# Performance work log

Measured on AMD Instinct MI355X. Metric: run time of the kernel, lower is better.

Reference implementation:

```python
import jax, jax.numpy as jnp
import numpy as np

FEAT = 1152
HID = [768, 512, 256]
WS = 32
LN_EPS = 1e-5


def _ln(x, g, b):
    mu = jnp.mean(x, axis=-1, keepdims=True)
    var = jnp.mean(jnp.square(x - mu), axis=-1, keepdims=True)
    return (x - mu) * jax.lax.rsqrt(var + LN_EPS) * g + b


def setup_inputs() -> dict:
    key = jax.random.key(0)
    ks = jax.random.split(key, 16)
    B, N, C = 8, 9216, FEAT

    def lin(k, din, dout):
        s = 1.0 / np.sqrt(din)
        k1, k2 = jax.random.split(k)
        return (jax.random.uniform(k1, (din, dout), jnp.float32, -s, s),
                jax.random.uniform(k2, (dout,), jnp.float32, -s, s))

    x = jax.random.normal(ks[0], (B, N, C), jnp.float32)
    W1, b1 = lin(ks[1], C, HID[0])
    W2, b2 = lin(ks[2], HID[0], HID[1])
    W3, b3 = lin(ks[3], HID[1], HID[2])
    Wo, bo = lin(ks[4], HID[2], C)
    red = C // 8
    ca_w1, ca_b1 = lin(ks[5], C, red)
    ca_w2, ca_b2 = lin(ks[6], red, C)
    return {
        "x": x,
        "W1": W1, "b1": b1, "g1": jnp.ones((HID[0],)), "be1": jnp.zeros((HID[0],)),
        "W2": W2, "b2": b2, "g2": jnp.ones((HID[1],)), "be2": jnp.zeros((HID[1],)),
        "W3": W3, "b3": b3, "g3": jnp.ones((HID[2],)), "be3": jnp.zeros((HID[2],)),
        "Wo": Wo, "bo": bo,
        "ca_w1": ca_w1, "ca_b1": ca_b1, "ca_w2": ca_w2, "ca_b2": ca_b2,
    }


def reference(x, W1, b1, g1, be1, W2, b2, g2, be2, W3, b3, g3, be3,
              Wo, bo, ca_w1, ca_b1, ca_w2, ca_b2):
    B, N, C = x.shape
    # projection + hidden blocks: Linear -> GELU(exact) -> LayerNorm
    h = _ln(jax.nn.gelu(x @ W1 + b1, approximate=False), g1, be1)
    h = _ln(jax.nn.gelu(h @ W2 + b2, approximate=False), g2, be2)
    h = _ln(jax.nn.gelu(h @ W3 + b3, approximate=False), g3, be3)
    y = h @ Wo + bo  # (B, N, C)
    # SE channel attention: global avg-pool over seq, 1x1 convs (=linear)
    pooled = jnp.mean(y, axis=1)                                  # (B, C)
    s = jax.nn.relu(pooled @ ca_w1 + ca_b1)                       # (B, C/8)
    s = jax.nn.sigmoid(s @ ca_w2 + ca_b2)                         # (B, C)
    y = y * s[:, None, :]
    # block-diagonal local self-attention, window = WS, scale 1/sqrt(C)
    nw = N // WS
    yw = y.reshape(B, nw, WS, C)
    scores = jnp.einsum('bwqc,bwkc->bwqk', yw, yw) / jnp.sqrt(jnp.asarray(C, y.dtype))
    attn = jax.nn.softmax(scores, axis=-1)
    out = jnp.einsum('bwqk,bwkc->bwqc', attn, yw)
    return out.reshape(B, N, C)
```

## Files before the change

### kernel.cpp

```cpp
#include <hip/hip_runtime.h>
#include <cstdint>
#include <cstddef>

typedef __bf16 bf16;
typedef __bf16 bf16x8 __attribute__((ext_vector_type(8)));
typedef float f32x4 __attribute__((ext_vector_type(4)));

__device__ __forceinline__ void gload_lds16(const bf16* g, bf16* l) {
    __builtin_amdgcn_global_load_lds((const __attribute__((address_space(1))) void*)g,
                                     (__attribute__((address_space(3))) void*)l, 16, 0, 0);
}

__global__ void cvt_f32_bf16_kernel(const float* __restrict__ in, bf16* __restrict__ outp, size_t n) {
    const size_t i = ((size_t)blockIdx.x * 256 + threadIdx.x) * 8;
    if (i >= n) return;
    const float4 a = *(const float4*)(in + i);
    const float4 b = *(const float4*)(in + i + 4);
    bf16x8 o;
    o[0] = (bf16)a.x; o[1] = (bf16)a.y; o[2] = (bf16)a.z; o[3] = (bf16)a.w;
    o[4] = (bf16)b.x; o[5] = (bf16)b.y; o[6] = (bf16)b.z; o[7] = (bf16)b.w;
    *(bf16x8*)(outp + i) = o;
}

__global__ void wtrans_all_kernel(const float* __restrict__ W1, bf16* __restrict__ T1,
                                  const float* __restrict__ W2, bf16* __restrict__ T2,
                                  const float* __restrict__ W3, bf16* __restrict__ T3,
                                  const float* __restrict__ Wo, bf16* __restrict__ To)
{
    __shared__ bf16 tile[64][65];
    const int id = blockIdx.x;
    const int t = threadIdx.x;
    const float* W; bf16* T; int K, N, kb, nb;
    if (id < 216)      { W = W1; T = T1; K = 1152; N = 768;  const int r = id;       kb = r % 18; nb = r / 18; }
    else if (id < 312) { W = W2; T = T2; K = 768;  N = 512;  const int r = id - 216; kb = r % 12; nb = r / 12; }
    else if (id < 344) { W = W3; T = T3; K = 512;  N = 256;  const int r = id - 312; kb = r % 8;  nb = r / 8;  }
    else               { W = Wo; T = To; K = 256;  N = 1152; const int r = id - 344; kb = r % 4;  nb = r / 4;  }
    const int k0 = kb << 6;
    const int n0 = nb << 6;
#pragma unroll
    for (int i = 0; i < 16; ++i) {
        const int flat = i * 256 + t;
        const int r = flat >> 6;
        const int c = flat & 63;
        tile[c][r] = (bf16)W[(size_t)(k0 + r) * N + n0 + c];
    }
    __syncthreads();
#pragma unroll
    for (int i = 0; i < 16; ++i) {
        const int flat = i * 256 + t;
        const int r = flat >> 6;
        const int c = flat & 63;
        T[(size_t)(n0 + r) * K + k0 + c] = tile[r][c];
    }
}

__device__ __forceinline__ int xcd_swz(int bid, int nwg) {
    return (bid & 7) * (nwg >> 3) + (bid >> 3);
}

__global__ void gemm_bf16_kernel(const bf16* __restrict__ A, const bf16* __restrict__ Bt,
                                 const float* __restrict__ bias, bf16* __restrict__ C,
                                 int K, int N, int nx, int do_gelu)
{
    __shared__ bf16 Alds[128 * 64];
    __shared__ bf16 Blds[128 * 64];
    const int t = threadIdx.x;
    const int w = t >> 6;
    const int l = t & 63;
    const int l15 = l & 15, l4 = l >> 4;
    const int wgid = xcd_swz(blockIdx.x, gridDim.x);
    const int mblk = wgid / nx;
    const int nblk = wgid - mblk * nx;
    const int m0 = mblk << 7;
    const int n0 = nblk << 7;
    const int wm = (w >> 1) << 6;
    const int wn = (w & 1) << 6;

    f32x4 acc[4][4] = {};

    int sr[4], sg[4];
#pragma unroll
    for (int i = 0; i < 4; ++i) {
        const int flat = i * 256 + t;
        sr[i] = flat >> 3;
        sg[i] = ((flat & 7) ^ (sr[i] & 7)) << 3;
    }

    for (int k0 = 0; k0 < K; k0 += 64) {
#pragma unroll
        for (int i = 0; i < 4; ++i) {
            gload_lds16(A + (size_t)(m0 + sr[i]) * K + (k0 + sg[i]),
                        &Alds[(size_t)(i * 256 + (w << 6)) << 3]);
            gload_lds16(Bt + (size_t)(n0 + sr[i]) * K + (k0 + sg[i]),
                        &Blds[(size_t)(i * 256 + (w << 6)) << 3]);
        }
        __syncthreads();
#pragma unroll
        for (int kk = 0; kk < 2; ++kk) {
            bf16x8 af[4], bfv[4];
#pragma unroll
            for (int i = 0; i < 4; ++i) {
                const int r = wm + (i << 4) + l15;
                const int g = (kk << 2) + l4;
                af[i] = *(const bf16x8*)&Alds[(r << 6) + ((g ^ (r & 7)) << 3)];
                const int rn = wn + (i << 4) + l15;
                bfv[i] = *(const bf16x8*)&Blds[(rn << 6) + ((g ^ (rn & 7)) << 3)];
            }
#pragma unroll
            for (int i = 0; i < 4; ++i)
#pragma unroll
                for (int j = 0; j < 4; ++j)
                    acc[i][j] = __builtin_amdgcn_mfma_f32_16x16x32_bf16(af[i], bfv[j], acc[i][j], 0, 0, 0);
        }
        __syncthreads();
    }

#pragma unroll
    for (int i = 0; i < 4; ++i) {
        const int mb = m0 + wm + (i << 4) + (l4 << 2);
#pragma unroll
        for (int j = 0; j < 4; ++j) {
            const int col = n0 + wn + (j << 4) + l15;
            const float bv = bias[col];
#pragma unroll
            for (int r = 0; r < 4; ++r) {
                float v = acc[i][j][r] + bv;
                if (do_gelu) v = 0.5f * v * (1.0f + erff(v * 0.70710678118654752f));
                C[(size_t)(mb + r) * N + col] = (bf16)v;
            }
        }
    }
}

__global__ void ln768_kernel(bf16* __restrict__ H, const float* __restrict__ g,
                             const float* __restrict__ be)
{
    const int t = threadIdx.x;
    const int rloc = t >> 7;
    const int u = t & 127;
    bf16* hp = H + ((size_t)blockIdx.x * 2 + rloc) * 768;
    float v[8];
    float s1 = 0.f, s2 = 0.f;
    if (u < 96) {
        const bf16x8 hv = *(const bf16x8*)(hp + u * 8);
#pragma unroll
        for (int e = 0; e < 8; ++e) { v[e] = (float)hv[e]; s1 += v[e]; s2 += v[e] * v[e]; }
    }
#pragma unroll
    for (int m = 1; m < 64; m <<= 1) { s1 += __shfl_xor(s1, m, 64); s2 += __shfl_xor(s2, m, 64); }
    __shared__ float red[8];
    const int w = t >> 6;
    if ((t & 63) == 0) { red[w] = s1; red[w + 4] = s2; }
    __syncthreads();
    const int wb = rloc << 1;
    s1 = red[wb] + red[wb + 1];
    s2 = red[wb + 4] + red[wb + 5];
    const float mu = s1 * (1.0f / 768.0f);
    const float rstd = rsqrtf(s2 * (1.0f / 768.0f) - mu * mu + 1e-5f);
    if (u < 96) {
        const float4 g0 = *(const float4*)(g + u * 8);
        const float4 g1 = *(const float4*)(g + u * 8 + 4);
        const float4 b0 = *(const float4*)(be + u * 8);
        const float4 b1 = *(const float4*)(be + u * 8 + 4);
        bf16x8 o;
        o[0] = (bf16)((v[0] - mu) * rstd * g0.x + b0.x);
        o[1] = (bf16)((v[1] - mu) * rstd * g0.y + b0.y);
        o[2] = (bf16)((v[2] - mu) * rstd * g0.z + b0.z);
        o[3] = (bf16)((v[3] - mu) * rstd * g0.w + b0.w);
        o[4] = (bf16)((v[4] - mu) * rstd * g1.x + b1.x);
        o[5] = (bf16)((v[5] - mu) * rstd * g1.y + b1.y);
        o[6] = (bf16)((v[6] - mu) * rstd * g1.z + b1.z);
        o[7] = (bf16)((v[7] - mu) * rstd * g1.w + b1.w);
        *(bf16x8*)(hp + u * 8) = o;
    }
}

__global__ void ln512_kernel(bf16* __restrict__ H, const float* __restrict__ g,
                             const float* __restrict__ be)
{
    const int t = threadIdx.x;
    const int w = t >> 6, l = t & 63;
    bf16* hp = H + ((size_t)blockIdx.x * 4 + w) * 512;
    const bf16x8 hv = *(const bf16x8*)(hp + l * 8);
    float v[8];
    float s1 = 0.f, s2 = 0.f;
#pragma unroll
    for (int e = 0; e < 8; ++e) { v[e] = (float)hv[e]; s1 += v[e]; s2 += v[e] * v[e]; }
#pragma unroll
    for (int m = 1; m < 64; m <<= 1) { s1 += __shfl_xor(s1, m, 64); s2 += __shfl_xor(s2, m, 64); }
    const float mu = s1 * (1.0f / 512.0f);
    const float rstd = rsqrtf(s2 * (1.0f / 512.0f) - mu * mu + 1e-5f);
    const float4 g0 = *(const float4*)(g + l * 8);
    const float4 g1 = *(const float4*)(g + l * 8 + 4);
    const float4 b0 = *(const float4*)(be + l * 8);
    const float4 b1 = *(const float4*)(be + l * 8 + 4);
    bf16x8 o;
    o[0] = (bf16)((v[0] - mu) * rstd * g0.x + b0.x);
    o[1] = (bf16)((v[1] - mu) * rstd * g0.y + b0.y);
    o[2] = (bf16)((v[2] - mu) * rstd * g0.z + b0.z);
    o[3] = (bf16)((v[3] - mu) * rstd * g0.w + b0.w);
    o[4] = (bf16)((v[4] - mu) * rstd * g1.x + b1.x);
    o[5] = (bf16)((v[5] - mu) * rstd * g1.y + b1.y);
    o[6] = (bf16)((v[6] - mu) * rstd * g1.z + b1.z);
    o[7] = (bf16)((v[7] - mu) * rstd * g1.w + b1.w);
    *(bf16x8*)(hp + l * 8) = o;
}

__global__ void ln256_kernel(bf16* __restrict__ H, const float* __restrict__ g,
                             const float* __restrict__ be)
{
    const int t = threadIdx.x;
    const int rloc = t >> 5, l = t & 31;
    bf16* hp = H + ((size_t)blockIdx.x * 8 + rloc) * 256;
    const bf16x8 hv = *(const bf16x8*)(hp + l * 8);
    float v[8];
    float s1 = 0.f, s2 = 0.f;
#pragma unroll
    for (int e = 0; e < 8; ++e) { v[e] = (float)hv[e]; s1 += v[e]; s2 += v[e] * v[e]; }
#pragma unroll
    for (int m = 1; m < 32; m <<= 1) { s1 += __shfl_xor(s1, m, 64); s2 += __shfl_xor(s2, m, 64); }
    const float mu = s1 * (1.0f / 256.0f);
    const float rstd = rsqrtf(s2 * (1.0f / 256.0f) - mu * mu + 1e-5f);
    const float4 g0 = *(const float4*)(g + l * 8);
    const float4 g1 = *(const float4*)(g + l * 8 + 4);
    const float4 b0 = *(const float4*)(be + l * 8);
    const float4 b1 = *(const float4*)(be + l * 8 + 4);
    bf16x8 o;
    o[0] = (bf16)((v[0] - mu) * rstd * g0.x + b0.x);
    o[1] = (bf16)((v[1] - mu) * rstd * g0.y + b0.y);
    o[2] = (bf16)((v[2] - mu) * rstd * g0.z + b0.z);
    o[3] = (bf16)((v[3] - mu) * rstd * g0.w + b0.w);
    o[4] = (bf16)((v[4] - mu) * rstd * g1.x + b1.x);
    o[5] = (bf16)((v[5] - mu) * rstd * g1.y + b1.y);
    o[6] = (bf16)((v[6] - mu) * rstd * g1.z + b1.z);
    o[7] = (bf16)((v[7] - mu) * rstd * g1.w + b1.w);
    *(bf16x8*)(hp + l * 8) = o;
}

__global__ void pool1_kernel(const bf16* __restrict__ Y, float* __restrict__ ppart) {
    const int c = blockIdx.x * 128 + threadIdx.x;
    const int nc = blockIdx.y;
    const int b = blockIdx.z;
    const bf16* yp = Y + ((size_t)b * 9216 + (size_t)nc * 256) * 1152 + c;
    float s = 0.f;
#pragma unroll 4
    for (int i = 0; i < 256; ++i) s += (float)yp[(size_t)i * 1152];
    ppart[((size_t)b * 36 + nc) * 1152 + c] = s;
}

__global__ void se_kernel(const float* __restrict__ ppart,
                          const float* __restrict__ w1, const float* __restrict__ b1,
                          const float* __restrict__ w2, const float* __restrict__ b2,
                          float* __restrict__ sbuf)
{
    const int b = blockIdx.x, t = threadIdx.x;
    __shared__ float p[1152];
    __shared__ float t1[144];
    for (int c = t; c < 1152; c += 256) {
        float s = 0.f;
#pragma unroll
        for (int j = 0; j < 36; ++j) s += ppart[((size_t)b * 36 + j) * 1152 + c];
        p[c] = s * (1.0f / 9216.0f);
    }
    __syncthreads();
    if (t < 144) {
        float a = b1[t];
        for (int k = 0; k < 1152; ++k) a += p[k] * w1[k * 144 + t];
        t1[t] = a > 0.f ? a : 0.f;
    }
    __syncthreads();
    for (int c = t; c < 1152; c += 256) {
        float a = b2[c];
#pragma unroll 8
        for (int k = 0; k < 144; ++k) a += t1[k] * w2[k * 1152 + c];
        sbuf[b * 1152 + c] = 1.0f / (1.0f + expf(-a));
    }
}

__device__ __forceinline__ int fswz(int r) { return (r & 7) ^ ((r >> 3) & 3); }

#define OSTG_STRIDE 388

__global__ void attn_kernel(const bf16* __restrict__ Y, const float* __restrict__ sbuf,
                            float* __restrict__ out)
{
    __shared__ __align__(16) char smem[24576 + 49664 + 2048];
    bf16*  yw   = (bf16*)smem;
    float* SpF  = (float*)(smem + 24576);
    float* ostg = (float*)(smem + 24576);
    bf16*  P    = (bf16*)(smem + 24576 + 49664);

    const int t = threadIdx.x;
    const int w = t >> 6, l = t & 63;
    const int l15 = l & 15, l4 = l >> 4;
    const int wdx = blockIdx.x, b = blockIdx.y;

    const bf16* Yp = Y + ((size_t)b * 9216 + (size_t)wdx * 32) * 1152;
    const float* sv = sbuf + b * 1152;
    float* op = out + ((size_t)b * 9216 + (size_t)wdx * 32) * 1152;

    auto stage_chunk = [&](int cc) {
#pragma unroll
        for (int i = 0; i < 6; ++i) {
            const int flat = i * 256 + t;
            const int r = flat / 48;
            const int gg = flat - r * 48;
            const int c0 = cc * 384 + gg * 8;
            const bf16x8 yv = *(const bf16x8*)(Yp + (size_t)r * 1152 + c0);
            const float4 sa = *(const float4*)(sv + c0);
            const float4 sb = *(const float4*)(sv + c0 + 4);
            bf16x8 ov;
            ov[0] = (bf16)((float)yv[0] * sa.x);
            ov[1] = (bf16)((float)yv[1] * sa.y);
            ov[2] = (bf16)((float)yv[2] * sa.z);
            ov[3] = (bf16)((float)yv[3] * sa.w);
            ov[4] = (bf16)((float)yv[4] * sb.x);
            ov[5] = (bf16)((float)yv[5] * sb.y);
            ov[6] = (bf16)((float)yv[6] * sb.z);
            ov[7] = (bf16)((float)yv[7] * sb.w);
            *(bf16x8*)&yw[((r * 48) + (gg ^ fswz(r))) << 3] = ov;
        }
    };

    f32x4 acc[2][2] = {};
    for (int cc = 0; cc < 3; ++cc) {
        if (cc) __syncthreads();
        stage_chunk(cc);
        __syncthreads();
#pragma unroll
        for (int kkl = 0; kkl < 3; ++kkl) {
            const int g = ((w * 3 + kkl) << 2) + l4;
            bf16x8 af[2];
#pragma unroll
            for (int i = 0; i < 2; ++i) {
                const int r = (i << 4) + l15;
                af[i] = *(const bf16x8*)&yw[((r * 48) + (g ^ fswz(r))) << 3];
            }
#pragma unroll
            for (int i = 0; i < 2; ++i)
#pragma unroll
                for (int j = 0; j < 2; ++j)
                    acc[i][j] = __builtin_amdgcn_mfma_f32_16x16x32_bf16(af[i], af[j], acc[i][j], 0, 0, 0);
        }
    }
#pragma unroll
    for (int i = 0; i < 2; ++i)
#pragma unroll
        for (int j = 0; j < 2; ++j)
#pragma unroll
            for (int r = 0; r < 4; ++r)
                SpF[w * 1056 + ((i << 4) + (l4 << 2) + r) * 33 + (j << 4) + l15] = acc[i][j][r];
    __syncthreads();

    {
        const int q = t >> 3, u = t & 7;
        float v[4];
#pragma unroll
        for (int e = 0; e < 4; ++e) {
            const int k2 = (u << 2) + e;
            v[e] = (SpF[q * 33 + k2] + SpF[1056 + q * 33 + k2] +
                    SpF[2112 + q * 33 + k2] + SpF[3168 + q * 33 + k2]) * 0.029462782549439483f;
        }
        float mx = fmaxf(fmaxf(v[0], v[1]), fmaxf(v[2], v[3]));
#pragma unroll
        for (int m = 1; m < 8; m <<= 1) mx = fmaxf(mx, __shfl_xor(mx, m, 64));
        float sm = 0.f;
#pragma unroll
        for (int e = 0; e < 4; ++e) { v[e] = expf(v[e] - mx); sm += v[e]; }
#pragma unroll
        for (int m = 1; m < 8; m <<= 1) sm += __shfl_xor(sm, m, 64);
        const float inv = 1.0f / sm;
#pragma unroll
        for (int e = 0; e < 4; ++e) P[(q << 5) + (u << 2) + e] = (bf16)(v[e] * inv);
    }
    __syncthreads();

    bf16x8 pa[2];
#pragma unroll
    for (int i = 0; i < 2; ++i)
        pa[i] = *(const bf16x8*)&P[(((i << 4) + l15) << 5) + (l4 << 3)];

    for (int ci = 0; ci < 3; ++ci) {
        const int cc = (ci == 0) ? 2 : (ci - 1);
        if (ci) {
            __syncthreads();
            stage_chunk(cc);
            __syncthreads();
        }
        f32x4 pacc[2][6] = {};
#pragma unroll
        for (int jn = 0; jn < 6; ++jn) {
            const int nl = w * 96 + (jn << 4) + l15;
            const int gg = nl >> 3, e = nl & 7;
            bf16x8 bv;
#pragma unroll
            for (int j = 0; j < 8; ++j) {
                const int kr = (l4 << 3) + j;
                bv[j] = yw[(((kr * 48) + (gg ^ fswz(kr))) << 3) + e];
            }
#pragma unroll
            for (int i = 0; i < 2; ++i)
                pacc[i][jn] = __builtin_amdgcn_mfma_f32_16x16x32_bf16(pa[i], bv, pacc[i][jn], 0, 0, 0);
        }
#pragma unroll
        for (int i = 0; i < 2; ++i)
#pragma unroll
            for (int jn = 0; jn < 6; ++jn)
#pragma unroll
                for (int r = 0; r < 4; ++r)
                    ostg[((i << 4) + (l4 << 2) + r) * OSTG_STRIDE + w * 96 + (jn << 4) + l15] =
                        pacc[i][jn][r];
        __syncthreads();
        {
            const int row = t >> 3;
            const int cb = (t & 7) << 2;
            float* orow = op + (size_t)row * 1152 + cc * 384;
            const float* srow = &ostg[row * OSTG_STRIDE];
#pragma unroll
            for (int k2 = 0; k2 < 12; ++k2) {
                const int c = cb + (k2 << 5);
                *(float4*)(orow + c) = *(const float4*)(srow + c);
            }
        }
        if (ci < 2) continue;
    }
}

extern "C" void kernel_launch(void* const* d_in, const int* in_sizes, int n_in,
                              void* d_out, int out_size, void* d_ws, size_t ws_size,
                              hipStream_t stream)
{
    const float* x   = (const float*)d_in[0];
    const float* W1  = (const float*)d_in[1];
    const float* b1  = (const float*)d_in[2];
    const float* g1  = (const float*)d_in[3];
    const float* be1 = (const float*)d_in[4];
    const float* W2  = (const float*)d_in[5];
    const float* b2  = (const float*)d_in[6];
    const float* g2  = (const float*)d_in[7];
    const float* be2 = (const float*)d_in[8];
    const float* W3  = (const float*)d_in[9];
    const float* b3  = (const float*)d_in[10];
    const float* g3  = (const float*)d_in[11];
    const float* be3 = (const float*)d_in[12];
    const float* Wo  = (const float*)d_in[13];
    const float* bo  = (const float*)d_in[14];
    const float* cw1 = (const float*)d_in[15];
    const float* cb1 = (const float*)d_in[16];
    const float* cw2 = (const float*)d_in[17];
    const float* cb2 = (const float*)d_in[18];
    float* out = (float*)d_out;

    const int M = 8 * 9216;
    size_t off = 0;
    auto alloc = [&](size_t nbytes) {
        void* p = (char*)d_ws + off;
        off += (nbytes + 255) & ~(size_t)255;
        return p;
    };
    bf16* Yb  = (bf16*)alloc((size_t)M * 1152 * 2);
    bf16* Hb  = (bf16*)alloc((size_t)M * 768 * 2);
    bf16* H2  = (bf16*)alloc((size_t)M * 512 * 2);
    bf16* Wt1 = (bf16*)alloc(768ull * 1152 * 2);
    bf16* Wt2 = (bf16*)alloc(512ull * 768 * 2);
    bf16* Wt3 = (bf16*)alloc(256ull * 512 * 2);
    bf16* Wto = (bf16*)alloc(1152ull * 256 * 2);
    float* ppart = (float*)alloc(8ull * 36 * 1152 * 4);
    float* sbuf  = (float*)alloc(8ull * 1152 * 4);
    bf16* Xb = Yb;
    bf16* H1 = Hb;
    bf16* H3 = Hb;

    cvt_f32_bf16_kernel<<<41472, 256, 0, stream>>>(x, Xb, (size_t)M * 1152);
    wtrans_all_kernel<<<416, 256, 0, stream>>>(W1, Wt1, W2, Wt2, W3, Wt3, Wo, Wto);

    gemm_bf16_kernel<<<6 * 576, 256, 0, stream>>>(Xb, Wt1, b1, H1, 1152, 768, 6, 1);
    ln768_kernel<<<M / 2, 256, 0, stream>>>(H1, g1, be1);
    gemm_bf16_kernel<<<4 * 576, 256, 0, stream>>>(H1, Wt2, b2, H2, 768, 512, 4, 1);
    ln512_kernel<<<M / 4, 256, 0, stream>>>(H2, g2, be2);
    gemm_bf16_kernel<<<2 * 576, 256, 0, stream>>>(H2, Wt3, b3, H3, 512, 256, 2, 1);
    ln256_kernel<<<M / 8, 256, 0, stream>>>(H3, g3, be3);
    gemm_bf16_kernel<<<9 * 576, 256, 0, stream>>>(H3, Wto, bo, Yb, 256, 1152, 9, 0);

    pool1_kernel<<<dim3(9, 36, 8), 128, 0, stream>>>(Yb, ppart);
    se_kernel<<<8, 256, 0, stream>>>(ppart, cw1, cb1, cw2, cb2, sbuf);
    attn_kernel<<<dim3(288, 8), 256, 0, stream>>>(Yb, sbuf, out);
}
```

Measured before the change: 884.1 us.

## Fuse sequence mean-pool into output GEMM epilogue and halve attention staging LDS

The output projection GEMM now reduces its fp32 accumulators per column inside each 128-row tile and writes partial sums (with bias folded in) to a 576-row partial buffer, removing the separate pool1 pass that re-read the whole bf16 Y tensor. The SE kernel now sums 72 partials per batch instead of 36. Separately, the attention kernel's output staging is split into two 16-row halves so the fp32 staging buffer in LDS is half as large, which may raise occupancy at the cost of extra barriers. Pooling from fp32 accumulators also slightly changes numerics compared with summing rounded bf16 values.

```diff
diff --git a/kernel.cpp b/kernel.cpp
--- a/kernel.cpp
+++ b/kernel.cpp
@@ -60,10 +60,12 @@
 
 __global__ void gemm_bf16_kernel(const bf16* __restrict__ A, const bf16* __restrict__ Bt,
                                  const float* __restrict__ bias, bf16* __restrict__ C,
-                                 int K, int N, int nx, int do_gelu)
+                                 int K, int N, int nx, int do_gelu,
+                                 float* __restrict__ ppart)
 {
     __shared__ bf16 Alds[128 * 64];
     __shared__ bf16 Blds[128 * 64];
+    __shared__ float psum[2][128];
     const int t = threadIdx.x;
     const int w = t >> 6;
     const int l = t & 63;
@@ -128,6 +130,25 @@
                 if (do_gelu) v = 0.5f * v * (1.0f + erff(v * 0.70710678118654752f));
                 C[(size_t)(mb + r) * N + col] = (bf16)v;
             }
+        }
+    }
+
+    if (ppart) {
+#pragma unroll
+        for (int j = 0; j < 4; ++j) {
+            float cs = 0.f;
+#pragma unroll
+            for (int i = 0; i < 4; ++i)
+#pragma unroll
+                for (int r = 0; r < 4; ++r) cs += acc[i][j][r];
+            cs += __shfl_xor(cs, 16, 64);
+            cs += __shfl_xor(cs, 32, 64);
+            if (l4 == 0) psum[w >> 1][((w & 1) << 6) + (j << 4) + l15] = cs;
+        }
+        __syncthreads();
+        if (t < 128) {
+            const int col = n0 + t;
+            ppart[(size_t)mblk * N + col] = psum[0][t] + psum[1][t] + 128.0f * bias[col];
         }
     }
 }
@@ -237,17 +258,6 @@
     *(bf16x8*)(hp + l * 8) = o;
 }
 
-__global__ void pool1_kernel(const bf16* __restrict__ Y, float* __restrict__ ppart) {
-    const int c = blockIdx.x * 128 + threadIdx.x;
-    const int nc = blockIdx.y;
-    const int b = blockIdx.z;
-    const bf16* yp = Y + ((size_t)b * 9216 + (size_t)nc * 256) * 1152 + c;
-    float s = 0.f;
-#pragma unroll 4
-    for (int i = 0; i < 256; ++i) s += (float)yp[(size_t)i * 1152];
-    ppart[((size_t)b * 36 + nc) * 1152 + c] = s;
-}
-
 __global__ void se_kernel(const float* __restrict__ ppart,
                           const float* __restrict__ w1, const float* __restrict__ b1,
                           const float* __restrict__ w2, const float* __restrict__ b2,
@@ -258,8 +268,8 @@
     __shared__ float t1[144];
     for (int c = t; c < 1152; c += 256) {
         float s = 0.f;
-#pragma unroll
-        for (int j = 0; j < 36; ++j) s += ppart[((size_t)b * 36 + j) * 1152 + c];
+#pragma unroll 8
+        for (int j = 0; j < 72; ++j) s += ppart[(size_t)(b * 72 + j) * 1152 + c];
         p[c] = s * (1.0f / 9216.0f);
     }
     __syncthreads();
@@ -284,11 +294,11 @@
 __global__ void attn_kernel(const bf16* __restrict__ Y, const float* __restrict__ sbuf,
                             float* __restrict__ out)
 {
-    __shared__ __align__(16) char smem[24576 + 49664 + 2048];
+    __shared__ __align__(16) char smem[24576 + 24832 + 2048];
     bf16*  yw   = (bf16*)smem;
     float* SpF  = (float*)(smem + 24576);
     float* ostg = (float*)(smem + 24576);
-    bf16*  P    = (bf16*)(smem + 24576 + 49664);
+    bf16*  P    = (bf16*)(smem + 24576 + 24832);
 
     const int t = threadIdx.x;
     const int w = t >> 6, l = t & 63;
@@ -403,26 +413,28 @@
                 pacc[i][jn] = __builtin_amdgcn_mfma_f32_16x16x32_bf16(pa[i], bv, pacc[i][jn], 0, 0, 0);
         }
 #pragma unroll
-        for (int i = 0; i < 2; ++i)
+        for (int half = 0; half < 2; ++half) {
+            if (half) __syncthreads();
 #pragma unroll
             for (int jn = 0; jn < 6; ++jn)
 #pragma unroll
                 for (int r = 0; r < 4; ++r)
-                    ostg[((i << 4) + (l4 << 2) + r) * OSTG_STRIDE + w * 96 + (jn << 4) + l15] =
-                        pacc[i][jn][r];
-        __syncthreads();
-        {
-            const int row = t >> 3;
-            const int cb = (t & 7) << 2;
-            float* orow = op + (size_t)row * 1152 + cc * 384;
-            const float* srow = &ostg[row * OSTG_STRIDE];
-#pragma unroll
-            for (int k2 = 0; k2 < 12; ++k2) {
-                const int c = cb + (k2 << 5);
-                *(float4*)(orow + c) = *(const float4*)(srow + c);
+                    ostg[((l4 << 2) + r) * OSTG_STRIDE + w * 96 + (jn << 4) + l15] =
+                        pacc[half][jn][r];
+            __syncthreads();
+            {
+                const int row = t >> 4;
+                const int cb = (t & 15) << 2;
+                float* orow = op + (size_t)(row + (half << 4)) * 1152 + cc * 384;
+                const float* srow = &ostg[row * OSTG_STRIDE];
+#pragma unroll
+                for (int k2 = 0; k2 < 6; ++k2) {
+                    const int c = cb + (k2 << 6);
+                    *(float4*)(orow + c) = *(const float4*)(srow + c);
+                }
             }
         }
-        if (ci < 2) continue;
+        if (ci < 2) __syncthreads();
     }
 }
 
@@ -465,7 +477,7 @@
     bf16* Wt2 = (bf16*)alloc(512ull * 768 * 2);
     bf16* Wt3 = (bf16*)alloc(256ull * 512 * 2);
     bf16* Wto = (bf16*)alloc(1152ull * 256 * 2);
-    float* ppart = (float*)alloc(8ull * 36 * 1152 * 4);
+    float* ppart = (float*)alloc(576ull * 1152 * 4);
     float* sbuf  = (float*)alloc(8ull * 1152 * 4);
     bf16* Xb = Yb;
     bf16* H1 = Hb;
@@ -474,15 +486,14 @@
     cvt_f32_bf16_kernel<<<41472, 256, 0, stream>>>(x, Xb, (size_t)M * 1152);
     wtrans_all_kernel<<<416, 256, 0, stream>>>(W1, Wt1, W2, Wt2, W3, Wt3, Wo, Wto);
 
-    gemm_bf16_kernel<<<6 * 576, 256, 0, stream>>>(Xb, Wt1, b1, H1, 1152, 768, 6, 1);
+    gemm_bf16_kernel<<<6 * 576, 256, 0, stream>>>(Xb, Wt1, b1, H1, 1152, 768, 6, 1, nullptr);
     ln768_kernel<<<M / 2, 256, 0, stream>>>(H1, g1, be1);
-    gemm_bf16_kernel<<<4 * 576, 256, 0, stream>>>(H1, Wt2, b2, H2, 768, 512, 4, 1);
+    gemm_bf16_kernel<<<4 * 576, 256, 0, stream>>>(H1, Wt2, b2, H2, 768, 512, 4, 1, nullptr);
     ln512_kernel<<<M / 4, 256, 0, stream>>>(H2, g2, be2);
-    gemm_bf16_kernel<<<2 * 576, 256, 0, stream>>>(H2, Wt3, b3, H3, 512, 256, 2, 1);
+    gemm_bf16_kernel<<<2 * 576, 256, 0, stream>>>(H2, Wt3, b3, H3, 512, 256, 2, 1, nullptr);
     ln256_kernel<<<M / 8, 256, 0, stream>>>(H3, g3, be3);
-    gemm_bf16_kernel<<<9 * 576, 256, 0, stream>>>(H3, Wto, bo, Yb, 256, 1152, 9, 0);
-
-    pool1_kernel<<<dim3(9, 36, 8), 128, 0, stream>>>(Yb, ppart);
+    gemm_bf16_kernel<<<9 * 576, 256, 0, stream>>>(H3, Wto, bo, Yb, 256, 1152, 9, 0, ppart);
+
     se_kernel<<<8, 256, 0, stream>>>(ppart, cw1, cb1, cw2, cb2, sbuf);
     attn_kernel<<<dim3(288, 8), 256, 0, stream>>>(Yb, sbuf, out);
 }
```

Result: faster. 822.0 us (-7.0%).
